# Optimization experiments

Measured on AMD Instinct MI355X. Metric: run time of the kernel, lower is better.

## Reference

```python
import jax, jax.numpy as jnp
import numpy as np

MASK_OD = np.array([
    [False, False, False, True, True, True, True, False, False],
    [False, False, True, True, True, True, True, True, False],
    [False, True, True, True, True, True, True, True, True],
    [True, True, True, True, True, True, True, False, True],
    [True, True, True, True, True, True, True, False, True],
    [False, True, True, True, True, True, True, True, True],
    [False, False, True, True, True, True, True, True, False],
    [False, False, False, True, True, True, True, False, False]], dtype=bool)

SCALE = float(np.sqrt(128.0))  # sqrt(attn_dim)


def build_prior(num_points=52):
    # Faithful reproduction of _init_anatomical_prior (OD laterality, no flip)
    pr_grid = np.arange(196) // 14
    pc_grid = np.arange(196) % 14
    prior = np.zeros((num_points, 196), dtype=np.float32)
    vf_idx = 0
    for r in range(8):
        for c in range(9):
            if MASK_OD[r, c]:
                pr = 13 - int(r * 13 / 7)
                pc = 13 - int(c * 13 / 8)
                prior[vf_idx] = -((pr_grid - pr) ** 2 + (pc_grid - pc) ** 2) / (2.0 * 3.0 ** 2)
                vf_idx += 1
    return prior


def setup_inputs() -> dict:
    key = jax.random.key(0)
    ks = jax.random.split(key, 8)
    B, P, K, E, A = 256, 52, 196, 1024, 128
    return {
        "patches": jax.random.normal(ks[0], (B, K, E), jnp.float32),
        "queries": jax.random.normal(ks[1], (P, A), jnp.float32) * 0.02,
        "Wk": jax.random.normal(ks[2], (A, E), jnp.float32) / np.sqrt(E),
        "Wv": jax.random.normal(ks[3], (A, E), jnp.float32) / np.sqrt(E),
        "Wo": jax.random.normal(ks[4], (E, A), jnp.float32) / np.sqrt(A),
        "bo": jnp.zeros((E,), jnp.float32),
        "patch_pos": jax.random.normal(ks[5], (K, A), jnp.float32) * 0.02,
        "temperature": jnp.asarray(2.0, jnp.float32),
        "attn_prior": jnp.asarray(build_prior(P)),
    }


def reference(patches, queries, Wk, Wv, Wo, bo, patch_pos, temperature, attn_prior):
    # patches: [B, 196, E]; laterality fixed to 'OD' (no prior flip)
    keys = jnp.einsum('bke,ae->bka', patches, Wk) + patch_pos  # [B, 196, A]
    vals = jnp.einsum('bke,ae->bka', patches, Wv)              # [B, 196, A]
    logits = jnp.einsum('qa,bka->bqk', queries, keys) / SCALE  # [B, 52, 196]
    temp = jax.nn.softplus(temperature) + 0.5
    logits = (logits + attn_prior[None]) / temp
    attn_weights = jax.nn.softmax(logits, axis=-1)
    # dropout is identity in eval mode
    attended = jnp.einsum('bqk,bka->bqa', attn_weights, vals)  # [B, 52, A]
    out = jnp.einsum('bqa,ea->bqe', attended, Wo) + bo         # [B, 52, E]
    return out, attn_weights
```

## Files before the change

### kernel.cpp

```cpp
#include <hip/hip_runtime.h>

typedef __attribute__((ext_vector_type(8))) short bf16x8;
typedef __attribute__((ext_vector_type(4))) short bf16x4;
typedef __attribute__((ext_vector_type(4))) float f32x4;
typedef __attribute__((ext_vector_type(4))) float floatx4;

__device__ __forceinline__ unsigned short f2bf(float f) {
    unsigned int u = __float_as_uint(f);
    u += 0x7fffu + ((u >> 16) & 1u);
    return (unsigned short)(u >> 16);
}
__device__ __forceinline__ float bf2f_s(short h) {
    return __uint_as_float(((unsigned int)(unsigned short)h) << 16);
}

__global__ void k_convert(const float* __restrict__ Wk, const float* __restrict__ Wv,
                          const float* __restrict__ Wo,
                          unsigned short* __restrict__ Wkvb, unsigned short* __restrict__ Wob) {
    int i = blockIdx.x * blockDim.x + threadIdx.x;
    if (i < 131072) {
        Wkvb[i]          = f2bf(Wk[i]);
        Wkvb[131072 + i] = f2bf(Wv[i]);
        Wob[i]           = f2bf(Wo[i]);
    }
}

__global__ __launch_bounds__(512)
void k_keysvals(const float* __restrict__ patches,
                const unsigned short* __restrict__ Wkvb,
                const float* __restrict__ patch_pos,
                unsigned short* __restrict__ kv)
{
    __shared__ unsigned short As[64][72];
    __shared__ unsigned short Bs[256][72];

    const int tid  = threadIdx.x;
    const int lane = tid & 63;
    const int wave = tid >> 6;
    const int wm   = wave >> 2;
    const int wn   = wave & 3;
    const int l15  = lane & 15;
    const int lg   = lane >> 4;
    const int row0 = blockIdx.x * 64;

    f32x4 acc[2][4];
    #pragma unroll
    for (int i = 0; i < 2; ++i)
        #pragma unroll
        for (int j = 0; j < 4; ++j)
            acc[i][j] = (f32x4){0.f, 0.f, 0.f, 0.f};

    for (int ko = 0; ko < 1024; ko += 64) {
        {
            int r = tid >> 4;
            int c = (tid & 15) * 4;
            #pragma unroll
            for (int it = 0; it < 2; ++it) {
                floatx4 v = *reinterpret_cast<const floatx4*>(
                    patches + (size_t)(row0 + it * 32 + r) * 1024 + ko + c);
                bf16x4 sv;
                sv[0] = (short)f2bf(v[0]); sv[1] = (short)f2bf(v[1]);
                sv[2] = (short)f2bf(v[2]); sv[3] = (short)f2bf(v[3]);
                *reinterpret_cast<bf16x4*>(&As[it * 32 + r][c]) = sv;
            }
        }
        {
            int r = tid >> 3;
            int c = (tid & 7) * 8;
            #pragma unroll
            for (int it = 0; it < 4; ++it) {
                bf16x8 v = *reinterpret_cast<const bf16x8*>(
                    Wkvb + (size_t)(it * 64 + r) * 1024 + ko + c);
                *reinterpret_cast<bf16x8*>(&Bs[it * 64 + r][c]) = v;
            }
        }
        __syncthreads();
        #pragma unroll
        for (int kk = 0; kk < 2; ++kk) {
            bf16x8 af[2], bfr[4];
            #pragma unroll
            for (int mi = 0; mi < 2; ++mi)
                af[mi] = *reinterpret_cast<const bf16x8*>(&As[wm * 32 + mi * 16 + l15][kk * 32 + lg * 8]);
            #pragma unroll
            for (int ni = 0; ni < 4; ++ni)
                bfr[ni] = *reinterpret_cast<const bf16x8*>(&Bs[wn * 64 + ni * 16 + l15][kk * 32 + lg * 8]);
            #pragma unroll
            for (int mi = 0; mi < 2; ++mi)
                #pragma unroll
                for (int ni = 0; ni < 4; ++ni)
                    acc[mi][ni] = __builtin_amdgcn_mfma_f32_16x16x32_bf16(af[mi], bfr[ni], acc[mi][ni], 0, 0, 0);
        }
        __syncthreads();
    }
    #pragma unroll
    for (int mi = 0; mi < 2; ++mi) {
        #pragma unroll
        for (int i = 0; i < 4; ++i) {
            int m  = row0 + wm * 32 + mi * 16 + lg * 4 + i;
            int kp = m % 196;
            #pragma unroll
            for (int ni = 0; ni < 4; ++ni) {
                int n = wn * 64 + ni * 16 + l15;
                float v = acc[mi][ni][i];
                if (n < 128) v += patch_pos[kp * 128 + n];
                kv[(size_t)m * 256 + n] = f2bf(v);
            }
        }
    }
}

__global__ __launch_bounds__(1024)
void k_attn(const unsigned short* __restrict__ kv,
            const float* __restrict__ queries,
            const float* __restrict__ prior,
            const float* __restrict__ temperature,
            float* __restrict__ attn_out,
            unsigned short* __restrict__ att)
{
    __shared__ unsigned short k_s[196][136];
    __shared__ unsigned short v_s[196][128];
    __shared__ unsigned short q_s[52][128];
    __shared__ float          l_s[52][196];

    const int b   = blockIdx.x;
    const int tid = threadIdx.x;
    const size_t base = (size_t)b * 196 * 256;

    for (int idx = tid; idx < 6272; idx += 1024) {
        int row = idx >> 5;
        int c   = (idx & 31) * 8;
        bf16x8 v = *reinterpret_cast<const bf16x8*>(kv + base + row * 256 + c);
        if (c < 128) *reinterpret_cast<bf16x8*>(&k_s[row][c])       = v;
        else         *reinterpret_cast<bf16x8*>(&v_s[row][c - 128]) = v;
    }
    for (int idx = tid; idx < 1664; idx += 1024) {
        int row = idx >> 5;
        int c   = (idx & 31) * 4;
        const float* qp = queries + row * 128 + c;
        bf16x4 sv;
        sv[0] = (short)f2bf(qp[0]); sv[1] = (short)f2bf(qp[1]);
        sv[2] = (short)f2bf(qp[2]); sv[3] = (short)f2bf(qp[3]);
        *reinterpret_cast<bf16x4*>(&q_s[row][c]) = sv;
    }
    __syncthreads();

    const float inv_temp  = 1.0f / (log1pf(expf(temperature[0])) + 0.5f);
    const float inv_scale = 0.08838834764831845f;

    for (int task = tid; task < 3328; task += 1024) {
        int q  = task >> 6;
        int kg = task & 63;
        if (kg < 49) {
            float dot0 = 0.f, dot1 = 0.f, dot2 = 0.f, dot3 = 0.f;
            #pragma unroll 4
            for (int c = 0; c < 128; c += 8) {
                bf16x8 qv = *reinterpret_cast<const bf16x8*>(&q_s[q][c]);
                float qf[8];
                #pragma unroll
                for (int e = 0; e < 8; ++e) qf[e] = bf2f_s(qv[e]);
                bf16x8 k0v = *reinterpret_cast<const bf16x8*>(&k_s[kg][c]);
                bf16x8 k1v = *reinterpret_cast<const bf16x8*>(&k_s[kg + 49][c]);
                bf16x8 k2v = *reinterpret_cast<const bf16x8*>(&k_s[kg + 98][c]);
                bf16x8 k3v = *reinterpret_cast<const bf16x8*>(&k_s[kg + 147][c]);
                #pragma unroll
                for (int e = 0; e < 8; ++e) {
                    dot0 += qf[e] * bf2f_s(k0v[e]);
                    dot1 += qf[e] * bf2f_s(k1v[e]);
                    dot2 += qf[e] * bf2f_s(k2v[e]);
                    dot3 += qf[e] * bf2f_s(k3v[e]);
                }
            }
            int k;
            k = kg;       l_s[q][k] = (dot0 * inv_scale + prior[q * 196 + k]) * inv_temp;
            k = kg + 49;  l_s[q][k] = (dot1 * inv_scale + prior[q * 196 + k]) * inv_temp;
            k = kg + 98;  l_s[q][k] = (dot2 * inv_scale + prior[q * 196 + k]) * inv_temp;
            k = kg + 147; l_s[q][k] = (dot3 * inv_scale + prior[q * 196 + k]) * inv_temp;
        }
    }
    __syncthreads();

    const int lane = tid & 63;
    const int wave = tid >> 6;
    for (int q = wave; q < 52; q += 16) {
        float x0 = l_s[q][lane];
        float x1 = l_s[q][lane + 64];
        float x2 = l_s[q][lane + 128];
        float x3 = (lane < 4) ? l_s[q][lane + 192] : -1e30f;
        float m = fmaxf(fmaxf(x0, x1), fmaxf(x2, x3));
        #pragma unroll
        for (int off = 32; off > 0; off >>= 1) m = fmaxf(m, __shfl_xor(m, off));
        float e0 = expf(x0 - m), e1 = expf(x1 - m), e2 = expf(x2 - m);
        float e3 = (lane < 4) ? expf(x3 - m) : 0.0f;
        float s = e0 + e1 + e2 + e3;
        #pragma unroll
        for (int off = 32; off > 0; off >>= 1) s += __shfl_xor(s, off);
        float inv = 1.0f / s;
        float* po = attn_out + ((size_t)b * 52 + q) * 196;
        float a0 = e0 * inv, a1 = e1 * inv, a2 = e2 * inv;
        l_s[q][lane]       = a0;  po[lane]       = a0;
        l_s[q][lane + 64]  = a1;  po[lane + 64]  = a1;
        l_s[q][lane + 128] = a2;  po[lane + 128] = a2;
        if (lane < 4) { float a3 = e3 * inv; l_s[q][lane + 192] = a3; po[lane + 192] = a3; }
    }
    __syncthreads();

    if (tid < 832) {
        int q  = tid >> 4;
        int a0 = (tid & 15) * 8;
        float accv[8] = {0.f, 0.f, 0.f, 0.f, 0.f, 0.f, 0.f, 0.f};
        for (int k = 0; k < 196; ++k) {
            float w = l_s[q][k];
            bf16x8 vv = *reinterpret_cast<const bf16x8*>(&v_s[k][a0]);
            #pragma unroll
            for (int e = 0; e < 8; ++e) accv[e] += w * bf2f_s(vv[e]);
        }
        bf16x8 sv;
        #pragma unroll
        for (int e = 0; e < 8; ++e) sv[e] = (short)f2bf(accv[e]);
        *reinterpret_cast<bf16x8*>(att + ((size_t)b * 52 + q) * 128 + a0) = sv;
    }
}

__global__ __launch_bounds__(512)
void k_out(const unsigned short* __restrict__ att,
           const unsigned short* __restrict__ Wob,
           const float* __restrict__ bo,
           float* __restrict__ out)
{
    __shared__ unsigned short As[64][72];
    __shared__ unsigned short Bs[256][72];

    const int tid  = threadIdx.x;
    const int lane = tid & 63;
    const int wave = tid >> 6;
    const int wm   = wave >> 2;
    const int wn   = wave & 3;
    const int l15  = lane & 15;
    const int lg   = lane >> 4;
    const int row0 = blockIdx.x * 64;
    const int e0   = blockIdx.y * 256;

    f32x4 acc[2][4];
    #pragma unroll
    for (int i = 0; i < 2; ++i)
        #pragma unroll
        for (int j = 0; j < 4; ++j)
            acc[i][j] = (f32x4){0.f, 0.f, 0.f, 0.f};

    for (int ko = 0; ko < 128; ko += 64) {
        {
            int r = tid >> 3;
            int c = (tid & 7) * 8;
            bf16x8 v = *reinterpret_cast<const bf16x8*>(att + (size_t)(row0 + r) * 128 + ko + c);
            *reinterpret_cast<bf16x8*>(&As[r][c]) = v;
        }
        {
            int r = tid >> 3;
            int c = (tid & 7) * 8;
            #pragma unroll
            for (int it = 0; it < 4; ++it) {
                bf16x8 v = *reinterpret_cast<const bf16x8*>(Wob + (size_t)(e0 + it * 64 + r) * 128 + ko + c);
                *reinterpret_cast<bf16x8*>(&Bs[it * 64 + r][c]) = v;
            }
        }
        __syncthreads();
        #pragma unroll
        for (int kk = 0; kk < 2; ++kk) {
            bf16x8 af[2], bfr[4];
            #pragma unroll
            for (int mi = 0; mi < 2; ++mi)
                af[mi] = *reinterpret_cast<const bf16x8*>(&As[wm * 32 + mi * 16 + l15][kk * 32 + lg * 8]);
            #pragma unroll
            for (int ni = 0; ni < 4; ++ni)
                bfr[ni] = *reinterpret_cast<const bf16x8*>(&Bs[wn * 64 + ni * 16 + l15][kk * 32 + lg * 8]);
            #pragma unroll
            for (int mi = 0; mi < 2; ++mi)
                #pragma unroll
                for (int ni = 0; ni < 4; ++ni)
                    acc[mi][ni] = __builtin_amdgcn_mfma_f32_16x16x32_bf16(af[mi], bfr[ni], acc[mi][ni], 0, 0, 0);
        }
        __syncthreads();
    }
    #pragma unroll
    for (int mi = 0; mi < 2; ++mi) {
        #pragma unroll
        for (int i = 0; i < 4; ++i) {
            int m = row0 + wm * 32 + mi * 16 + lg * 4 + i;
            #pragma unroll
            for (int ni = 0; ni < 4; ++ni) {
                int e = e0 + wn * 64 + ni * 16 + l15;
                out[(size_t)m * 1024 + e] = acc[mi][ni][i] + bo[e];
            }
        }
    }
}

extern "C" void kernel_launch(void* const* d_in, const int* in_sizes, int n_in,
                              void* d_out, int out_size, void* d_ws, size_t ws_size,
                              hipStream_t stream)
{
    const float* patches     = (const float*)d_in[0];
    const float* queries     = (const float*)d_in[1];
    const float* Wk          = (const float*)d_in[2];
    const float* Wv          = (const float*)d_in[3];
    const float* Wo          = (const float*)d_in[4];
    const float* bo          = (const float*)d_in[5];
    const float* patch_pos   = (const float*)d_in[6];
    const float* temperature = (const float*)d_in[7];
    const float* prior       = (const float*)d_in[8];

    float* out      = (float*)d_out;
    float* attn_out = out + (size_t)256 * 52 * 1024;

    unsigned short* Wkvb = (unsigned short*)d_ws;
    unsigned short* Wob  = Wkvb + 256 * 1024;
    unsigned short* kv   = Wob + 1024 * 128;
    unsigned short* att  = kv + (size_t)50176 * 256;

    k_convert <<<512, 256, 0, stream>>>(Wk, Wv, Wo, Wkvb, Wob);
    k_keysvals<<<784, 512, 0, stream>>>(patches, Wkvb, patch_pos, kv);
    k_attn    <<<256, 1024, 0, stream>>>(kv, queries, prior, temperature, attn_out, att);
    k_out     <<<dim3(208, 4), 512, 0, stream>>>(att, Wob, bo, out);
}
```

Measured before the change: 161.6 us.

## Stream K/V GEMM tiles via direct global-to-LDS loads with XOR swizzle

The keys/values GEMM now loads fp32 patch tiles and bf16 weight tiles straight into LDS with global_load_lds, using XOR-swizzled layouts to avoid bank conflicts. The fp32-to-bf16 conversion moves to fragment-read time with packed cvt instructions. The GEMM is split into two N-halves per 64-row tile (256-thread blocks, twice as many blocks), and the weight-conversion kernel is vectorised. This removes the register round-trip and in-loop conversion on the load path, but doubles LDS bytes for A and re-reads the patches for each N half.

```diff
diff --git a/kernel.cpp b/kernel.cpp
--- a/kernel.cpp
+++ b/kernel.cpp
@@ -14,34 +14,73 @@
     return __uint_as_float(((unsigned int)(unsigned short)h) << 16);
 }
 
+__device__ __forceinline__ void gload_lds16(const void* gsrc, void* ldst) {
+    __builtin_amdgcn_global_load_lds(
+        (const __attribute__((address_space(1))) unsigned int*)gsrc,
+        (__attribute__((address_space(3))) unsigned int*)ldst, 16, 0, 0);
+}
+
+__device__ __forceinline__ bf16x8 cvt8(f32x4 lo, f32x4 hi) {
+    union { unsigned int u[4]; bf16x8 v; } r;
+    asm("v_cvt_pk_bf16_f32 %0, %1, %2" : "=v"(r.u[0]) : "v"(lo[0]), "v"(lo[1]));
+    asm("v_cvt_pk_bf16_f32 %0, %1, %2" : "=v"(r.u[1]) : "v"(lo[2]), "v"(lo[3]));
+    asm("v_cvt_pk_bf16_f32 %0, %1, %2" : "=v"(r.u[2]) : "v"(hi[0]), "v"(hi[1]));
+    asm("v_cvt_pk_bf16_f32 %0, %1, %2" : "=v"(r.u[3]) : "v"(hi[2]), "v"(hi[3]));
+    return r.v;
+}
+
 __global__ void k_convert(const float* __restrict__ Wk, const float* __restrict__ Wv,
                           const float* __restrict__ Wo,
                           unsigned short* __restrict__ Wkvb, unsigned short* __restrict__ Wob) {
-    int i = blockIdx.x * blockDim.x + threadIdx.x;
+    int i = (blockIdx.x * blockDim.x + threadIdx.x) * 4;
     if (i < 131072) {
-        Wkvb[i]          = f2bf(Wk[i]);
-        Wkvb[131072 + i] = f2bf(Wv[i]);
-        Wob[i]           = f2bf(Wo[i]);
-    }
-}
-
-__global__ __launch_bounds__(512)
+        floatx4 a = *reinterpret_cast<const floatx4*>(Wk + i);
+        floatx4 b = *reinterpret_cast<const floatx4*>(Wv + i);
+        floatx4 c = *reinterpret_cast<const floatx4*>(Wo + i);
+        bf16x4 sa, sb, sc;
+        #pragma unroll
+        for (int e = 0; e < 4; ++e) {
+            sa[e] = (short)f2bf(a[e]); sb[e] = (short)f2bf(b[e]); sc[e] = (short)f2bf(c[e]);
+        }
+        *reinterpret_cast<bf16x4*>(Wkvb + i)          = sa;
+        *reinterpret_cast<bf16x4*>(Wkvb + 131072 + i) = sb;
+        *reinterpret_cast<bf16x4*>(Wob + i)           = sc;
+    }
+}
+
+__global__ __launch_bounds__(256, 4)
 void k_keysvals(const float* __restrict__ patches,
                 const unsigned short* __restrict__ Wkvb,
                 const float* __restrict__ patch_pos,
                 unsigned short* __restrict__ kv)
 {
-    __shared__ unsigned short As[64][72];
-    __shared__ unsigned short Bs[256][72];
+    __shared__ float          As[64 * 64];
+    __shared__ unsigned short Bs[128 * 64];
 
     const int tid  = threadIdx.x;
     const int lane = tid & 63;
     const int wave = tid >> 6;
-    const int wm   = wave >> 2;
-    const int wn   = wave & 3;
+    const int wm   = wave >> 1;
+    const int wn   = wave & 1;
     const int l15  = lane & 15;
     const int lg   = lane >> 4;
-    const int row0 = blockIdx.x * 64;
+
+    const int bid  = blockIdx.x;
+    const int nb   = bid & 1;
+    const int mt   = bid >> 1;
+    const int row0 = mt * 64;
+    const int n0   = nb * 128;
+
+    const int arow = tid >> 4;
+    const int agn  = (tid & 15) ^ arow;
+    const char* agbase = (const char*)(patches + (size_t)(row0 + arow) * 1024) + agn * 16;
+
+    const int brow = tid >> 3;
+    const int bgn  = (tid & 7) ^ (brow & 7);
+    const char* bgbase = (const char*)(Wkvb + (size_t)(n0 + brow) * 1024) + bgn * 16;
+
+    char* alds = (char*)As + tid * 16;
+    char* blds = (char*)Bs + tid * 16;
 
     f32x4 acc[2][4];
     #pragma unroll
@@ -50,48 +89,42 @@
         for (int j = 0; j < 4; ++j)
             acc[i][j] = (f32x4){0.f, 0.f, 0.f, 0.f};
 
-    for (int ko = 0; ko < 1024; ko += 64) {
-        {
-            int r = tid >> 4;
-            int c = (tid & 15) * 4;
-            #pragma unroll
-            for (int it = 0; it < 2; ++it) {
-                floatx4 v = *reinterpret_cast<const floatx4*>(
-                    patches + (size_t)(row0 + it * 32 + r) * 1024 + ko + c);
-                bf16x4 sv;
-                sv[0] = (short)f2bf(v[0]); sv[1] = (short)f2bf(v[1]);
-                sv[2] = (short)f2bf(v[2]); sv[3] = (short)f2bf(v[3]);
-                *reinterpret_cast<bf16x4*>(&As[it * 32 + r][c]) = sv;
-            }
-        }
-        {
-            int r = tid >> 3;
-            int c = (tid & 7) * 8;
-            #pragma unroll
-            for (int it = 0; it < 4; ++it) {
-                bf16x8 v = *reinterpret_cast<const bf16x8*>(
-                    Wkvb + (size_t)(it * 64 + r) * 1024 + ko + c);
-                *reinterpret_cast<bf16x8*>(&Bs[it * 64 + r][c]) = v;
-            }
-        }
+    for (int t = 0; t < 16; ++t) {
+        const int koA = t * 256;
+        const int koB = t * 128;
+        #pragma unroll
+        for (int i = 0; i < 4; ++i)
+            gload_lds16(agbase + (size_t)i * 65536 + koA, alds + i * 4096);
+        #pragma unroll
+        for (int i = 0; i < 4; ++i)
+            gload_lds16(bgbase + (size_t)i * 65536 + koB, blds + i * 4096);
         __syncthreads();
+
         #pragma unroll
         for (int kk = 0; kk < 2; ++kk) {
-            bf16x8 af[2], bfr[4];
-            #pragma unroll
-            for (int mi = 0; mi < 2; ++mi)
-                af[mi] = *reinterpret_cast<const bf16x8*>(&As[wm * 32 + mi * 16 + l15][kk * 32 + lg * 8]);
-            #pragma unroll
-            for (int ni = 0; ni < 4; ++ni)
-                bfr[ni] = *reinterpret_cast<const bf16x8*>(&Bs[wn * 64 + ni * 16 + l15][kk * 32 + lg * 8]);
-            #pragma unroll
-            for (int mi = 0; mi < 2; ++mi)
+            bf16x8 af[2];
+            #pragma unroll
+            for (int mi = 0; mi < 2; ++mi) {
+                const int mrow = wm * 32 + mi * 16 + l15;
+                const int q0   = (kk * 8 + lg * 2) ^ l15;
+                const int q1   = q0 ^ 1;
+                f32x4 lo = *reinterpret_cast<const f32x4*>((const char*)As + mrow * 256 + q0 * 16);
+                f32x4 hi = *reinterpret_cast<const f32x4*>((const char*)As + mrow * 256 + q1 * 16);
+                af[mi] = cvt8(lo, hi);
+            }
+            #pragma unroll
+            for (int ni = 0; ni < 4; ++ni) {
+                const int nrow = wn * 64 + ni * 16 + l15;
+                const int qb   = (kk * 4 + lg) ^ (l15 & 7);
+                bf16x8 bf = *reinterpret_cast<const bf16x8*>((const char*)Bs + nrow * 128 + qb * 16);
                 #pragma unroll
-                for (int ni = 0; ni < 4; ++ni)
-                    acc[mi][ni] = __builtin_amdgcn_mfma_f32_16x16x32_bf16(af[mi], bfr[ni], acc[mi][ni], 0, 0, 0);
+                for (int mi = 0; mi < 2; ++mi)
+                    acc[mi][ni] = __builtin_amdgcn_mfma_f32_16x16x32_bf16(af[mi], bf, acc[mi][ni], 0, 0, 0);
+            }
         }
         __syncthreads();
     }
+
     #pragma unroll
     for (int mi = 0; mi < 2; ++mi) {
         #pragma unroll
@@ -100,7 +133,7 @@
             int kp = m % 196;
             #pragma unroll
             for (int ni = 0; ni < 4; ++ni) {
-                int n = wn * 64 + ni * 16 + l15;
+                int n = n0 + wn * 64 + ni * 16 + l15;
                 float v = acc[mi][ni][i];
                 if (n < 128) v += patch_pos[kp * 128 + n];
                 kv[(size_t)m * 256 + n] = f2bf(v);
@@ -317,8 +350,8 @@
     unsigned short* kv   = Wob + 1024 * 128;
     unsigned short* att  = kv + (size_t)50176 * 256;
 
-    k_convert <<<512, 256, 0, stream>>>(Wk, Wv, Wo, Wkvb, Wob);
-    k_keysvals<<<784, 512, 0, stream>>>(patches, Wkvb, patch_pos, kv);
+    k_convert <<<128, 256, 0, stream>>>(Wk, Wv, Wo, Wkvb, Wob);
+    k_keysvals<<<1568, 256, 0, stream>>>(patches, Wkvb, patch_pos, kv);
     k_attn    <<<256, 1024, 0, stream>>>(kv, queries, prior, temperature, attn_out, att);
     k_out     <<<dim3(208, 4), 512, 0, stream>>>(att, Wob, bo, out);
 }
```

After: 158.9 us. About the same (-1.7%).

## Load GEMM operands directly from global into registers, dropping LDS staging and weight pre-conversion

Applied to the files above, without the earlier changes.

The keys/values GEMM no longer stages tiles in shared memory. Each wave now loads fp32 patches and fp32 Wk/Wv fragments straight from global memory into registers and converts them with packed bf16 conversion instructions. The separate Wk/Wv bf16 conversion pass is removed, the block shrinks to 4 waves each computing a 64x64 tile, and the Wo conversion is vectorized. This removes the LDS traffic, barriers and a pre-pass. In exchange, every wave rereads the full 64-row patch tile from global/L2 with scattered 32-byte accesses, and the weights are reconverted in every block.

```diff
diff --git a/kernel.cpp b/kernel.cpp
--- a/kernel.cpp
+++ b/kernel.cpp
@@ -14,95 +14,97 @@
     return __uint_as_float(((unsigned int)(unsigned short)h) << 16);
 }
 
-__global__ void k_convert(const float* __restrict__ Wk, const float* __restrict__ Wv,
-                          const float* __restrict__ Wo,
-                          unsigned short* __restrict__ Wkvb, unsigned short* __restrict__ Wob) {
-    int i = blockIdx.x * blockDim.x + threadIdx.x;
+__device__ __forceinline__ bf16x8 cvt8(f32x4 lo, f32x4 hi) {
+    union { unsigned int u[4]; bf16x8 v; } r;
+    asm("v_cvt_pk_bf16_f32 %0, %1, %2" : "=v"(r.u[0]) : "v"(lo[0]), "v"(lo[1]));
+    asm("v_cvt_pk_bf16_f32 %0, %1, %2" : "=v"(r.u[1]) : "v"(lo[2]), "v"(lo[3]));
+    asm("v_cvt_pk_bf16_f32 %0, %1, %2" : "=v"(r.u[2]) : "v"(hi[0]), "v"(hi[1]));
+    asm("v_cvt_pk_bf16_f32 %0, %1, %2" : "=v"(r.u[3]) : "v"(hi[2]), "v"(hi[3]));
+    return r.v;
+}
+
+__global__ void k_convert(const float* __restrict__ Wo, unsigned short* __restrict__ Wob) {
+    int i = (blockIdx.x * blockDim.x + threadIdx.x) * 4;
     if (i < 131072) {
-        Wkvb[i]          = f2bf(Wk[i]);
-        Wkvb[131072 + i] = f2bf(Wv[i]);
-        Wob[i]           = f2bf(Wo[i]);
-    }
-}
-
-__global__ __launch_bounds__(512)
+        floatx4 c = *reinterpret_cast<const floatx4*>(Wo + i);
+        bf16x4 sc;
+        #pragma unroll
+        for (int e = 0; e < 4; ++e) sc[e] = (short)f2bf(c[e]);
+        *reinterpret_cast<bf16x4*>(Wob + i) = sc;
+    }
+}
+
+__global__ __launch_bounds__(256, 2)
 void k_keysvals(const float* __restrict__ patches,
-                const unsigned short* __restrict__ Wkvb,
+                const float* __restrict__ Wk,
+                const float* __restrict__ Wv,
                 const float* __restrict__ patch_pos,
                 unsigned short* __restrict__ kv)
 {
-    __shared__ unsigned short As[64][72];
-    __shared__ unsigned short Bs[256][72];
-
     const int tid  = threadIdx.x;
     const int lane = tid & 63;
-    const int wave = tid >> 6;
-    const int wm   = wave >> 2;
-    const int wn   = wave & 3;
+    const int wn   = tid >> 6;
     const int l15  = lane & 15;
     const int lg   = lane >> 4;
     const int row0 = blockIdx.x * 64;
 
-    f32x4 acc[2][4];
-    #pragma unroll
-    for (int i = 0; i < 2; ++i)
+    const float* ap0 = patches + (size_t)(row0 +  0 + l15) * 1024 + lg * 8;
+    const float* ap1 = patches + (size_t)(row0 + 16 + l15) * 1024 + lg * 8;
+    const float* ap2 = patches + (size_t)(row0 + 32 + l15) * 1024 + lg * 8;
+    const float* ap3 = patches + (size_t)(row0 + 48 + l15) * 1024 + lg * 8;
+
+    const float* wsrc = (wn < 2) ? Wk : Wv;
+    const int    nloc = (wn & 1) * 64;
+    const float* bp0 = wsrc + (size_t)(nloc +  0 + l15) * 1024 + lg * 8;
+    const float* bp1 = wsrc + (size_t)(nloc + 16 + l15) * 1024 + lg * 8;
+    const float* bp2 = wsrc + (size_t)(nloc + 32 + l15) * 1024 + lg * 8;
+    const float* bp3 = wsrc + (size_t)(nloc + 48 + l15) * 1024 + lg * 8;
+
+    f32x4 acc[4][4];
+    #pragma unroll
+    for (int i = 0; i < 4; ++i)
         #pragma unroll
         for (int j = 0; j < 4; ++j)
             acc[i][j] = (f32x4){0.f, 0.f, 0.f, 0.f};
 
-    for (int ko = 0; ko < 1024; ko += 64) {
-        {
-            int r = tid >> 4;
-            int c = (tid & 15) * 4;
-            #pragma unroll
-            for (int it = 0; it < 2; ++it) {
-                floatx4 v = *reinterpret_cast<const floatx4*>(
-                    patches + (size_t)(row0 + it * 32 + r) * 1024 + ko + c);
-                bf16x4 sv;
-                sv[0] = (short)f2bf(v[0]); sv[1] = (short)f2bf(v[1]);
-                sv[2] = (short)f2bf(v[2]); sv[3] = (short)f2bf(v[3]);
-                *reinterpret_cast<bf16x4*>(&As[it * 32 + r][c]) = sv;
-            }
-        }
-        {
-            int r = tid >> 3;
-            int c = (tid & 7) * 8;
-            #pragma unroll
-            for (int it = 0; it < 4; ++it) {
-                bf16x8 v = *reinterpret_cast<const bf16x8*>(
-                    Wkvb + (size_t)(it * 64 + r) * 1024 + ko + c);
-                *reinterpret_cast<bf16x8*>(&Bs[it * 64 + r][c]) = v;
-            }
-        }
-        __syncthreads();
-        #pragma unroll
-        for (int kk = 0; kk < 2; ++kk) {
-            bf16x8 af[2], bfr[4];
-            #pragma unroll
-            for (int mi = 0; mi < 2; ++mi)
-                af[mi] = *reinterpret_cast<const bf16x8*>(&As[wm * 32 + mi * 16 + l15][kk * 32 + lg * 8]);
+    #pragma unroll
+    for (int t = 0; t < 32; ++t) {
+        const int o = t * 32;
+        bf16x8 af[4], bfr[4];
+        af[0] = cvt8(*reinterpret_cast<const f32x4*>(ap0 + o),
+                     *reinterpret_cast<const f32x4*>(ap0 + o + 4));
+        af[1] = cvt8(*reinterpret_cast<const f32x4*>(ap1 + o),
+                     *reinterpret_cast<const f32x4*>(ap1 + o + 4));
+        af[2] = cvt8(*reinterpret_cast<const f32x4*>(ap2 + o),
+                     *reinterpret_cast<const f32x4*>(ap2 + o + 4));
+        af[3] = cvt8(*reinterpret_cast<const f32x4*>(ap3 + o),
+                     *reinterpret_cast<const f32x4*>(ap3 + o + 4));
+        bfr[0] = cvt8(*reinterpret_cast<const f32x4*>(bp0 + o),
+                      *reinterpret_cast<const f32x4*>(bp0 + o + 4));
+        bfr[1] = cvt8(*reinterpret_cast<const f32x4*>(bp1 + o),
+                      *reinterpret_cast<const f32x4*>(bp1 + o + 4));
+        bfr[2] = cvt8(*reinterpret_cast<const f32x4*>(bp2 + o),
+                      *reinterpret_cast<const f32x4*>(bp2 + o + 4));
+        bfr[3] = cvt8(*reinterpret_cast<const f32x4*>(bp3 + o),
+                      *reinterpret_cast<const f32x4*>(bp3 + o + 4));
+        #pragma unroll
+        for (int mi = 0; mi < 4; ++mi)
             #pragma unroll
             for (int ni = 0; ni < 4; ++ni)
-                bfr[ni] = *reinterpret_cast<const bf16x8*>(&Bs[wn * 64 + ni * 16 + l15][kk * 32 + lg * 8]);
-            #pragma unroll
-            for (int mi = 0; mi < 2; ++mi)
-                #pragma unroll
-                for (int ni = 0; ni < 4; ++ni)
-                    acc[mi][ni] = __builtin_amdgcn_mfma_f32_16x16x32_bf16(af[mi], bfr[ni], acc[mi][ni], 0, 0, 0);
-        }
-        __syncthreads();
-    }
-    #pragma unroll
-    for (int mi = 0; mi < 2; ++mi) {
+                acc[mi][ni] = __builtin_amdgcn_mfma_f32_16x16x32_bf16(af[mi], bfr[ni], acc[mi][ni], 0, 0, 0);
+    }
+
+    #pragma unroll
+    for (int mi = 0; mi < 4; ++mi) {
         #pragma unroll
         for (int i = 0; i < 4; ++i) {
-            int m  = row0 + wm * 32 + mi * 16 + lg * 4 + i;
+            int m  = row0 + mi * 16 + lg * 4 + i;
             int kp = m % 196;
             #pragma unroll
             for (int ni = 0; ni < 4; ++ni) {
                 int n = wn * 64 + ni * 16 + l15;
                 float v = acc[mi][ni][i];
-                if (n < 128) v += patch_pos[kp * 128 + n];
+                if (wn < 2) v += patch_pos[kp * 128 + n];
                 kv[(size_t)m * 256 + n] = f2bf(v);
             }
         }
@@ -312,13 +314,12 @@
     float* out      = (float*)d_out;
     float* attn_out = out + (size_t)256 * 52 * 1024;
 
-    unsigned short* Wkvb = (unsigned short*)d_ws;
-    unsigned short* Wob  = Wkvb + 256 * 1024;
-    unsigned short* kv   = Wob + 1024 * 128;
-    unsigned short* att  = kv + (size_t)50176 * 256;
-
-    k_convert <<<512, 256, 0, stream>>>(Wk, Wv, Wo, Wkvb, Wob);
-    k_keysvals<<<784, 512, 0, stream>>>(patches, Wkvb, patch_pos, kv);
+    unsigned short* Wob = (unsigned short*)d_ws;
+    unsigned short* kv  = Wob + 1024 * 128;
+    unsigned short* att = kv + (size_t)50176 * 256;
+
+    k_convert <<<128, 256, 0, stream>>>(Wo, Wob);
+    k_keysvals<<<784, 256, 0, stream>>>(patches, Wk, Wv, patch_pos, kv);
     k_attn    <<<256, 1024, 0, stream>>>(kv, queries, prior, temperature, attn_out, att);
     k_out     <<<dim3(208, 4), 512, 0, stream>>>(att, Wob, bo, out);
 }
```

After: 360.1 us. 123% more time.

## Split K/V projection GEMM across blocks and convert weights inline

Applied to the files above, without the earlier changes.

The keys/values GEMM now gives each 256-thread block one 64x128 output tile (K or V half), doubling the grid. Each block reads fp32 Wk or Wv directly and converts to bf16 in the load path with packed cvt instructions, so the separate Wk/Wv conversion pass is removed and k_convert only handles Wo. The trade-off is that each patches tile is read and converted twice (once per half) and weights are converted repeatedly per block instead of once. Smaller blocks may raise occupancy.

```diff
diff --git a/kernel.cpp b/kernel.cpp
--- a/kernel.cpp
+++ b/kernel.cpp
@@ -14,34 +14,53 @@
     return __uint_as_float(((unsigned int)(unsigned short)h) << 16);
 }
 
-__global__ void k_convert(const float* __restrict__ Wk, const float* __restrict__ Wv,
-                          const float* __restrict__ Wo,
-                          unsigned short* __restrict__ Wkvb, unsigned short* __restrict__ Wob) {
-    int i = blockIdx.x * blockDim.x + threadIdx.x;
+__device__ __forceinline__ bf16x8 cvt8(f32x4 lo, f32x4 hi) {
+    union { unsigned int u[4]; bf16x8 v; } r;
+    asm("v_cvt_pk_bf16_f32 %0, %1, %2" : "=v"(r.u[0]) : "v"(lo[0]), "v"(lo[1]));
+    asm("v_cvt_pk_bf16_f32 %0, %1, %2" : "=v"(r.u[1]) : "v"(lo[2]), "v"(lo[3]));
+    asm("v_cvt_pk_bf16_f32 %0, %1, %2" : "=v"(r.u[2]) : "v"(hi[0]), "v"(hi[1]));
+    asm("v_cvt_pk_bf16_f32 %0, %1, %2" : "=v"(r.u[3]) : "v"(hi[2]), "v"(hi[3]));
+    return r.v;
+}
+
+__global__ void k_convert(const float* __restrict__ Wo, unsigned short* __restrict__ Wob) {
+    int i = (blockIdx.x * blockDim.x + threadIdx.x) * 4;
     if (i < 131072) {
-        Wkvb[i]          = f2bf(Wk[i]);
-        Wkvb[131072 + i] = f2bf(Wv[i]);
-        Wob[i]           = f2bf(Wo[i]);
-    }
-}
-
-__global__ __launch_bounds__(512)
+        floatx4 c = *reinterpret_cast<const floatx4*>(Wo + i);
+        bf16x4 sc;
+        #pragma unroll
+        for (int e = 0; e < 4; ++e) sc[e] = (short)f2bf(c[e]);
+        *reinterpret_cast<bf16x4*>(Wob + i) = sc;
+    }
+}
+
+__global__ __launch_bounds__(256)
 void k_keysvals(const float* __restrict__ patches,
-                const unsigned short* __restrict__ Wkvb,
+                const float* __restrict__ Wk,
+                const float* __restrict__ Wv,
                 const float* __restrict__ patch_pos,
                 unsigned short* __restrict__ kv)
 {
     __shared__ unsigned short As[64][72];
-    __shared__ unsigned short Bs[256][72];
+    __shared__ unsigned short Bs[128][72];
 
     const int tid  = threadIdx.x;
     const int lane = tid & 63;
     const int wave = tid >> 6;
-    const int wm   = wave >> 2;
-    const int wn   = wave & 3;
+    const int wm   = wave >> 1;
+    const int wn   = wave & 1;
     const int l15  = lane & 15;
     const int lg   = lane >> 4;
-    const int row0 = blockIdx.x * 64;
+
+    const int mt   = blockIdx.x >> 1;
+    const int nb   = blockIdx.x & 1;
+    const int row0 = mt * 64;
+    const float* wsrc = nb ? Wv : Wk;
+
+    const int ar = tid >> 2;
+    const int ac = (tid & 3) * 16;
+    const int br = tid >> 1;
+    const int bc = (tid & 1) * 32;
 
     f32x4 acc[2][4];
     #pragma unroll
@@ -52,27 +71,28 @@
 
     for (int ko = 0; ko < 1024; ko += 64) {
         {
-            int r = tid >> 4;
-            int c = (tid & 15) * 4;
-            #pragma unroll
-            for (int it = 0; it < 2; ++it) {
-                floatx4 v = *reinterpret_cast<const floatx4*>(
-                    patches + (size_t)(row0 + it * 32 + r) * 1024 + ko + c);
-                bf16x4 sv;
-                sv[0] = (short)f2bf(v[0]); sv[1] = (short)f2bf(v[1]);
-                sv[2] = (short)f2bf(v[2]); sv[3] = (short)f2bf(v[3]);
-                *reinterpret_cast<bf16x4*>(&As[it * 32 + r][c]) = sv;
-            }
+            const float* p = patches + (size_t)(row0 + ar) * 1024 + ko + ac;
+            f32x4 v0 = *reinterpret_cast<const f32x4*>(p);
+            f32x4 v1 = *reinterpret_cast<const f32x4*>(p + 4);
+            f32x4 v2 = *reinterpret_cast<const f32x4*>(p + 8);
+            f32x4 v3 = *reinterpret_cast<const f32x4*>(p + 12);
+            *reinterpret_cast<bf16x8*>(&As[ar][ac])     = cvt8(v0, v1);
+            *reinterpret_cast<bf16x8*>(&As[ar][ac + 8]) = cvt8(v2, v3);
         }
         {
-            int r = tid >> 3;
-            int c = (tid & 7) * 8;
-            #pragma unroll
-            for (int it = 0; it < 4; ++it) {
-                bf16x8 v = *reinterpret_cast<const bf16x8*>(
-                    Wkvb + (size_t)(it * 64 + r) * 1024 + ko + c);
-                *reinterpret_cast<bf16x8*>(&Bs[it * 64 + r][c]) = v;
-            }
+            const float* p = wsrc + (size_t)br * 1024 + ko + bc;
+            f32x4 v0 = *reinterpret_cast<const f32x4*>(p);
+            f32x4 v1 = *reinterpret_cast<const f32x4*>(p + 4);
+            f32x4 v2 = *reinterpret_cast<const f32x4*>(p + 8);
+            f32x4 v3 = *reinterpret_cast<const f32x4*>(p + 12);
+            f32x4 v4 = *reinterpret_cast<const f32x4*>(p + 16);
+            f32x4 v5 = *reinterpret_cast<const f32x4*>(p + 20);
+            f32x4 v6 = *reinterpret_cast<const f32x4*>(p + 24);
+            f32x4 v7 = *reinterpret_cast<const f32x4*>(p + 28);
+            *reinterpret_cast<bf16x8*>(&Bs[br][bc])      = cvt8(v0, v1);
+            *reinterpret_cast<bf16x8*>(&Bs[br][bc + 8])  = cvt8(v2, v3);
+            *reinterpret_cast<bf16x8*>(&Bs[br][bc + 16]) = cvt8(v4, v5);
+            *reinterpret_cast<bf16x8*>(&Bs[br][bc + 24]) = cvt8(v6, v7);
         }
         __syncthreads();
         #pragma unroll
@@ -92,6 +112,7 @@
         }
         __syncthreads();
     }
+
     #pragma unroll
     for (int mi = 0; mi < 2; ++mi) {
         #pragma unroll
@@ -100,9 +121,10 @@
             int kp = m % 196;
             #pragma unroll
             for (int ni = 0; ni < 4; ++ni) {
-                int n = wn * 64 + ni * 16 + l15;
+                int nl = wn * 64 + ni * 16 + l15;
+                int n  = nb * 128 + nl;
                 float v = acc[mi][ni][i];
-                if (n < 128) v += patch_pos[kp * 128 + n];
+                if (nb == 0) v += patch_pos[kp * 128 + nl];
                 kv[(size_t)m * 256 + n] = f2bf(v);
             }
         }
@@ -312,13 +334,12 @@
     float* out      = (float*)d_out;
     float* attn_out = out + (size_t)256 * 52 * 1024;
 
-    unsigned short* Wkvb = (unsigned short*)d_ws;
-    unsigned short* Wob  = Wkvb + 256 * 1024;
-    unsigned short* kv   = Wob + 1024 * 128;
-    unsigned short* att  = kv + (size_t)50176 * 256;
-
-    k_convert <<<512, 256, 0, stream>>>(Wk, Wv, Wo, Wkvb, Wob);
-    k_keysvals<<<784, 512, 0, stream>>>(patches, Wkvb, patch_pos, kv);
+    unsigned short* Wob = (unsigned short*)d_ws;
+    unsigned short* kv  = Wob + 1024 * 128;
+    unsigned short* att = kv + (size_t)50176 * 256;
+
+    k_convert <<<128, 256, 0, stream>>>(Wo, Wob);
+    k_keysvals<<<1568, 256, 0, stream>>>(patches, Wk, Wv, patch_pos, kv);
     k_attn    <<<256, 1024, 0, stream>>>(kv, queries, prior, temperature, attn_out, att);
     k_out     <<<dim3(208, 4), 512, 0, stream>>>(att, Wob, bo, out);
 }
```

After: 233.7 us. 1.45x slower.
